# Kernel optimization log

Hardware: AMD Instinct MI355X
Metric: run time of the kernel (lower is better)

## Reference

```python
import jax, jax.numpy as jnp
import numpy as np

KX = jnp.array([[1, 0, -1], [2, 0, -2], [1, 0, -1]], dtype=jnp.float32).reshape(1, 1, 3, 3)
KY = jnp.array([[1, 2, 1], [0, 0, 0], [-1, -2, -1]], dtype=jnp.float32).reshape(1, 1, 3, 3)


def setup_inputs() -> dict:
    key = jax.random.key(0)
    k1, k2 = jax.random.split(key)
    B, C, H, W = 32, 3, 512, 512
    sr = jax.random.uniform(k1, (B, C, H, W), dtype=jnp.float32)
    hr = jax.random.uniform(k2, (B, C, H, W), dtype=jnp.float32)
    return {"sr": sr, "hr": hr}


def _gray(x):
    # ITU-R 601 luma weights, NCHW -> [B,1,H,W]
    return 0.2989 * x[:, 0:1] + 0.587 * x[:, 1:2] + 0.114 * x[:, 2:3]


def _conv(x, k):
    # 1-channel 3x3 conv, padding=1 (SAME)
    return jax.lax.conv_general_dilated(
        x, k, window_strides=(1, 1), padding=((1, 1), (1, 1)),
        dimension_numbers=("NCHW", "OIHW", "NCHW"))


def reference(sr, hr):
    sr_g = _gray(sr)
    hr_g = _gray(hr)
    loss_x = jnp.mean(jnp.abs(_conv(sr_g, KX) - _conv(hr_g, KX)))
    loss_y = jnp.mean(jnp.abs(_conv(sr_g, KY) - _conv(hr_g, KY)))
    return loss_x + loss_y
```

## Files before the change

### kernel.cpp

```cpp
#include <hip/hip_runtime.h>


#define TH 8
#define TILE_ROWS (TH + 2)
#define ROWSTRIDE 516

__global__ __launch_bounds__(256, 8)
void edge_loss_kernel(const float* __restrict__ sr, const float* __restrict__ hr,
                      float* __restrict__ out) {
    __shared__ float tile[TILE_ROWS][ROWSTRIDE];
    const int tid   = threadIdx.x;
    const int img   = blockIdx.x >> 6;
    const int strip = blockIdx.x & 63;
    const int row0  = strip * TH;

    if (tid < TILE_ROWS) { tile[tid][0] = 0.f; tile[tid][513] = 0.f; }

    const size_t imgBase = (size_t)img * (3 * 512 * 512);
    const float* __restrict__ srp = sr + imgBase;
    const float* __restrict__ hrp = hr + imgBase;

    for (int idx = tid; idx < TILE_ROWS * 128; idx += 256) {
        const int r  = idx >> 7;
        const int x4 = (idx & 127) << 2;
        const int gr = row0 - 1 + r;
        float dx = 0.f, dy = 0.f, dz = 0.f, dw = 0.f;
        if (gr >= 0 && gr < 512) {
            const size_t off = (size_t)gr * 512 + x4;
            const float4 sR = *(const float4*)(srp + off);
            const float4 sG = *(const float4*)(srp + off + 262144);
            const float4 sB = *(const float4*)(srp + off + 524288);
            const float4 hR = *(const float4*)(hrp + off);
            const float4 hG = *(const float4*)(hrp + off + 262144);
            const float4 hB = *(const float4*)(hrp + off + 524288);
            dx = 0.2989f*(sR.x-hR.x) + 0.587f*(sG.x-hG.x) + 0.114f*(sB.x-hB.x);
            dy = 0.2989f*(sR.y-hR.y) + 0.587f*(sG.y-hG.y) + 0.114f*(sB.y-hB.y);
            dz = 0.2989f*(sR.z-hR.z) + 0.587f*(sG.z-hG.z) + 0.114f*(sB.z-hB.z);
            dw = 0.2989f*(sR.w-hR.w) + 0.587f*(sG.w-hG.w) + 0.114f*(sB.w-hB.w);
        }
        float* t = &tile[r][1 + x4];
        t[0] = dx; t[1] = dy; t[2] = dz; t[3] = dw;
    }
    __syncthreads();

    float acc = 0.f;
    #pragma unroll
    for (int i = 0; i < 4; ++i) {
        const int g  = tid + (i << 8);
        const int r  = g >> 7;
        const int x4 = (g & 127) << 2;
        const float* A  = &tile[r][x4];
        const float* Bc = &tile[r + 1][x4];
        const float* Cc = &tile[r + 2][x4];
        const float a0=A[0],a1=A[1],a2=A[2],a3=A[3],a4=A[4],a5=A[5];
        const float b0=Bc[0],b1=Bc[1],b2=Bc[2],b3=Bc[3],b4=Bc[4],b5=Bc[5];
        const float c0=Cc[0],c1=Cc[1],c2=Cc[2],c3=Cc[3],c4=Cc[4],c5=Cc[5];
        const float s0=a0+2.f*b0+c0, s1=a1+2.f*b1+c1, s2=a2+2.f*b2+c2,
                    s3=a3+2.f*b3+c3, s4=a4+2.f*b4+c4, s5=a5+2.f*b5+c5;
        acc += fabsf(s0 - s2) + fabsf(s1 - s3) + fabsf(s2 - s4) + fabsf(s3 - s5);
        acc += fabsf((a0 + 2.f*a1 + a2) - (c0 + 2.f*c1 + c2));
        acc += fabsf((a1 + 2.f*a2 + a3) - (c1 + 2.f*c2 + c3));
        acc += fabsf((a2 + 2.f*a3 + a4) - (c2 + 2.f*c3 + c4));
        acc += fabsf((a3 + 2.f*a4 + a5) - (c3 + 2.f*c4 + c5));
    }

    #pragma unroll
    for (int o = 32; o > 0; o >>= 1) acc += __shfl_down(acc, o, 64);
    __shared__ float wsum[4];
    if ((tid & 63) == 0) wsum[tid >> 6] = acc;
    __syncthreads();
    if (tid == 0) {
        const float s = (wsum[0] + wsum[1] + wsum[2] + wsum[3]) * (1.0f / 8388608.0f);
        atomicAdd(out, s);
    }
}

extern "C" void kernel_launch(void* const* d_in, const int* in_sizes, int n_in,
                              void* d_out, int out_size, void* d_ws, size_t ws_size,
                              hipStream_t stream) {
    const float* sr = (const float*)d_in[0];
    const float* hr = (const float*)d_in[1];
    float* out = (float*)d_out;
    hipMemsetAsync(out, 0, sizeof(float), stream);
    edge_loss_kernel<<<dim3(32 * 64), dim3(256), 0, stream>>>(sr, hr, out);
}
```

Measured before the change: 218.5 us.

## Split fused edge loss into grayscale-diff pass and Sobel reduction pass

Replaces the single fused tile kernel with two kernels when the workspace is large enough. The first computes the grayscale sr−hr difference with many independent float4 loads in flight per thread and writes a full-resolution intermediate buffer. The second applies both Sobel filters and reduces, using wave shuffles for horizontal neighbours instead of shared-memory tiles. The aim is more memory-level parallelism and no halo re-reads of the six input channels, at the cost of writing and re-reading a 32 MB intermediate plus a second launch. The old fused kernel is kept as a fallback when the workspace is too small.

```diff
diff --git a/kernel.cpp b/kernel.cpp
--- a/kernel.cpp
+++ b/kernel.cpp
@@ -1,25 +1,119 @@
 #include <hip/hip_runtime.h>
 
+
+__global__ __launch_bounds__(256, 4)
+void gray_diff_kernel(const float* __restrict__ sr, const float* __restrict__ hr,
+                      float* __restrict__ dd) {
+    const int t = blockIdx.x * 256 + threadIdx.x;
+    #pragma unroll
+    for (int half = 0; half < 2; ++half) {
+        float4 sR[4], sG[4], sB[4], hR[4], hG[4], hB[4];
+        #pragma unroll
+        for (int k = 0; k < 4; ++k) {
+            const int p   = t + (half * 4 + k) * 262144;
+            const int img = p >> 16;
+            const int g   = p & 65535;
+            const size_t base = (size_t)img * 786432 + ((size_t)g << 2);
+            sR[k] = *(const float4*)(sr + base);
+            sG[k] = *(const float4*)(sr + base + 262144);
+            sB[k] = *(const float4*)(sr + base + 524288);
+            hR[k] = *(const float4*)(hr + base);
+            hG[k] = *(const float4*)(hr + base + 262144);
+            hB[k] = *(const float4*)(hr + base + 524288);
+        }
+        #pragma unroll
+        for (int k = 0; k < 4; ++k) {
+            const int p = t + (half * 4 + k) * 262144;
+            float4 o;
+            o.x = 0.2989f*(sR[k].x-hR[k].x) + 0.587f*(sG[k].x-hG[k].x) + 0.114f*(sB[k].x-hB[k].x);
+            o.y = 0.2989f*(sR[k].y-hR[k].y) + 0.587f*(sG[k].y-hG[k].y) + 0.114f*(sB[k].y-hB[k].y);
+            o.z = 0.2989f*(sR[k].z-hR[k].z) + 0.587f*(sG[k].z-hG[k].z) + 0.114f*(sB[k].z-hB[k].z);
+            o.w = 0.2989f*(sR[k].w-hR[k].w) + 0.587f*(sG[k].w-hG[k].w) + 0.114f*(sB[k].w-hB[k].w);
+            *(float4*)(dd + ((size_t)p << 2)) = o;
+        }
+    }
+}
+
+__global__ __launch_bounds__(256, 8)
+void sobel_sum_kernel(const float* __restrict__ dd, float* __restrict__ out) {
+    const int tid  = threadIdx.x;
+    const int lane = tid & 63;
+    const int w    = tid >> 6;
+    const int img  = blockIdx.x >> 7;
+    const int rg   = blockIdx.x & 127;
+    const int y    = rg * 4 + w;
+    const float* base = dd + (size_t)img * 262144;
+    const int c0 = lane << 3;
+
+    float dm[8], dc[8], dp[8];
+    {
+        const float4 a = *(const float4*)(base + y * 512 + c0);
+        const float4 b = *(const float4*)(base + y * 512 + c0 + 4);
+        dc[0]=a.x; dc[1]=a.y; dc[2]=a.z; dc[3]=a.w; dc[4]=b.x; dc[5]=b.y; dc[6]=b.z; dc[7]=b.w;
+    }
+    if (y > 0) {
+        const float4 a = *(const float4*)(base + (y-1) * 512 + c0);
+        const float4 b = *(const float4*)(base + (y-1) * 512 + c0 + 4);
+        dm[0]=a.x; dm[1]=a.y; dm[2]=a.z; dm[3]=a.w; dm[4]=b.x; dm[5]=b.y; dm[6]=b.z; dm[7]=b.w;
+    } else {
+        #pragma unroll
+        for (int j = 0; j < 8; ++j) dm[j] = 0.f;
+    }
+    if (y < 511) {
+        const float4 a = *(const float4*)(base + (y+1) * 512 + c0);
+        const float4 b = *(const float4*)(base + (y+1) * 512 + c0 + 4);
+        dp[0]=a.x; dp[1]=a.y; dp[2]=a.z; dp[3]=a.w; dp[4]=b.x; dp[5]=b.y; dp[6]=b.z; dp[7]=b.w;
+    } else {
+        #pragma unroll
+        for (int j = 0; j < 8; ++j) dp[j] = 0.f;
+    }
+
+    float s[8], u[8];
+    #pragma unroll
+    for (int j = 0; j < 8; ++j) {
+        s[j] = dm[j] + 2.f * dc[j] + dp[j];
+        u[j] = dm[j] - dp[j];
+    }
+    float sL = __shfl_up(s[7], 1, 64);   if (lane == 0)  sL = 0.f;
+    float sR = __shfl_down(s[0], 1, 64); if (lane == 63) sR = 0.f;
+    float uL = __shfl_up(u[7], 1, 64);   if (lane == 0)  uL = 0.f;
+    float uR = __shfl_down(u[0], 1, 64); if (lane == 63) uR = 0.f;
+
+    float acc = 0.f;
+    acc += fabsf(sL - s[1]);
+    #pragma unroll
+    for (int j = 1; j < 7; ++j) acc += fabsf(s[j-1] - s[j+1]);
+    acc += fabsf(s[6] - sR);
+    acc += fabsf(uL + 2.f*u[0] + u[1]);
+    #pragma unroll
+    for (int j = 1; j < 7; ++j) acc += fabsf(u[j-1] + 2.f*u[j] + u[j+1]);
+    acc += fabsf(u[6] + 2.f*u[7] + uR);
+
+    #pragma unroll
+    for (int o = 32; o > 0; o >>= 1) acc += __shfl_down(acc, o, 64);
+    __shared__ float wsum[4];
+    if (lane == 0) wsum[w] = acc;
+    __syncthreads();
+    if (tid == 0)
+        atomicAdd(out, (wsum[0] + wsum[1] + wsum[2] + wsum[3]) * (1.0f / 8388608.0f));
+}
 
 #define TH 8
 #define TILE_ROWS (TH + 2)
 #define ROWSTRIDE 516
 
 __global__ __launch_bounds__(256, 8)
-void edge_loss_kernel(const float* __restrict__ sr, const float* __restrict__ hr,
-                      float* __restrict__ out) {
+void edge_loss_fused(const float* __restrict__ sr, const float* __restrict__ hr,
+                     float* __restrict__ out) {
     __shared__ float tile[TILE_ROWS][ROWSTRIDE];
     const int tid   = threadIdx.x;
     const int img   = blockIdx.x >> 6;
     const int strip = blockIdx.x & 63;
     const int row0  = strip * TH;
-
     if (tid < TILE_ROWS) { tile[tid][0] = 0.f; tile[tid][513] = 0.f; }
-
     const size_t imgBase = (size_t)img * (3 * 512 * 512);
     const float* __restrict__ srp = sr + imgBase;
     const float* __restrict__ hrp = hr + imgBase;
-
     for (int idx = tid; idx < TILE_ROWS * 128; idx += 256) {
         const int r  = idx >> 7;
         const int x4 = (idx & 127) << 2;
@@ -42,7 +136,6 @@
         t[0] = dx; t[1] = dy; t[2] = dz; t[3] = dw;
     }
     __syncthreads();
-
     float acc = 0.f;
     #pragma unroll
     for (int i = 0; i < 4; ++i) {
@@ -63,7 +156,6 @@
         acc += fabsf((a2 + 2.f*a3 + a4) - (c2 + 2.f*c3 + c4));
         acc += fabsf((a3 + 2.f*a4 + a5) - (c3 + 2.f*c4 + c5));
     }
-
     #pragma unroll
     for (int o = 32; o > 0; o >>= 1) acc += __shfl_down(acc, o, 64);
     __shared__ float wsum[4];
@@ -81,6 +173,13 @@
     const float* sr = (const float*)d_in[0];
     const float* hr = (const float*)d_in[1];
     float* out = (float*)d_out;
-    hipMemsetAsync(out, 0, sizeof(float), stream);
-    edge_loss_kernel<<<dim3(32 * 64), dim3(256), 0, stream>>>(sr, hr, out);
+    (void)hipMemsetAsync(out, 0, sizeof(float), stream);
+    const size_t needed = (size_t)32 * 512 * 512 * 4;
+    if (ws_size >= needed) {
+        float* dd = (float*)d_ws;
+        gray_diff_kernel<<<dim3(1024), dim3(256), 0, stream>>>(sr, hr, dd);
+        sobel_sum_kernel<<<dim3(4096), dim3(256), 0, stream>>>(dd, out);
+    } else {
+        edge_loss_fused<<<dim3(32 * 64), dim3(256), 0, stream>>>(sr, hr, out);
+    }
 }
```

After: 271.7 us. 1.24x slower.
